# Kernel optimization log

Hardware: AMD Instinct MI355X
Metric: run time of the kernel (lower is better)

The kernel has to match this reference:

```python
import jax, jax.numpy as jnp
import numpy as np

SEQ_LEN = 2_097_152  # free sequence dimension
NUM_SYMBOLS = 10
NUM_STATES = 10
NUM_CLASSES = 2


def setup_inputs() -> dict:
    key = jax.random.key(0)
    k1, k2, k3, k4 = jax.random.split(key, 4)
    # x[t] is a probability distribution over symbols (soft one-hot), matching
    # the automaton semantics and keeping the 2M-step recurrence numerically stable.
    x = jax.random.uniform(k1, (SEQ_LEN, NUM_SYMBOLS), dtype=jnp.float32)
    x = x / jnp.sum(x, axis=1, keepdims=True)
    # Parameters, initialized exactly as in the torch module (__init__ softmaxes).
    P = jax.nn.softmax(jax.random.normal(k2, (NUM_SYMBOLS, NUM_STATES, NUM_STATES), dtype=jnp.float32), axis=2)
    start_state = jax.nn.softmax(jax.random.normal(k3, (NUM_STATES,), dtype=jnp.float32), axis=0)
    accept_states = jax.nn.softmax(jax.random.normal(k4, (NUM_STATES, NUM_CLASSES), dtype=jnp.float32), axis=1)
    return {"x": x, "P": P, "start_state": start_state, "accept_states": accept_states}


def reference(x, P, start_state, accept_states):
    # Sequential recurrence: s_{t+1} = s_t @ (sum_k x[t,k] * P[k])
    def step(s, xt):
        Wt = jnp.einsum('k,kij->ij', xt, P)  # [S, S] symbol-weighted transition
        return s @ Wt, None
    s, _ = jax.lax.scan(step, start_state, x)
    return s @ accept_states  # [num_classes]
```

## Files before the change

### kernel.cpp

```cpp
#include <hip/hip_runtime.h>

#define TEN 10

__global__ __attribute__((amdgpu_flat_work_group_size(256, 256),
                          amdgpu_waves_per_eu(1, 1)))
void automaton_chunks(const float* __restrict__ x, const float* __restrict__ P,
                      float* __restrict__ outBlk, long long T, int C)
{
    __shared__ __align__(16) float lds[8704];

    const int tid  = threadIdx.x;
    const int wave = tid >> 6;
    const int lane = tid & 63;
    const int grp  = lane / 5;
    const int sub  = lane % 5;
    const bool active = (grp < 12);
    const int cib  = wave * 12 + grp;
    const int j0 = 2 * sub, j1 = j0 + 1;

    float p[2][TEN][TEN];
    float m[TEN][2];
    long long Lc = 0;
    const float2* xp = nullptr;
    float* slot = lds + (active ? cib : 0) * 132;

    if (active) {
        const long long chunk = (long long)blockIdx.x * 48 + cib;
        const long long s0 = chunk * T / C;
        const long long s1 = (chunk + 1) * T / C;
        Lc = s1 - s0;
        xp = reinterpret_cast<const float2*>(x) + s0 * 5;
#pragma unroll
        for (int k = 0; k < TEN; ++k)
#pragma unroll
            for (int a = 0; a < TEN; ++a) {
                const float2 v = *reinterpret_cast<const float2*>(P + k * 100 + a * TEN + j0);
                p[0][k][a] = v.x;
                p[1][k][a] = v.y;
            }
#pragma unroll
        for (int r = 0; r < TEN; ++r) {
            m[r][0] = (r == j0) ? 1.0f : 0.0f;
            m[r][1] = (r == j1) ? 1.0f : 0.0f;
        }
    }

    float2 nx0, nx1, nx2, nx3, nx4;
    if (active) { nx0 = xp[0]; nx1 = xp[1]; nx2 = xp[2]; nx3 = xp[3]; nx4 = xp[4]; xp += 5; }

    if (active) {
#pragma unroll 1
        for (long long s = 0; s < Lc; ++s) {
            const float xv[TEN] = {nx0.x, nx0.y, nx1.x, nx1.y, nx2.x,
                                   nx2.y, nx3.x, nx3.y, nx4.x, nx4.y};
            if (s + 1 < Lc) {
                nx0 = xp[0]; nx1 = xp[1]; nx2 = xp[2]; nx3 = xp[3]; nx4 = xp[4];
                xp += 5;
            }

            {
                float* c0 = slot + j0 * 12;
                reinterpret_cast<float4*>(c0)[0] = make_float4(m[0][0], m[1][0], m[2][0], m[3][0]);
                reinterpret_cast<float4*>(c0)[1] = make_float4(m[4][0], m[5][0], m[6][0], m[7][0]);
                reinterpret_cast<float2*>(c0 + 8)[0] = make_float2(m[8][0], m[9][0]);
                float* c1 = slot + j1 * 12;
                reinterpret_cast<float4*>(c1)[0] = make_float4(m[0][1], m[1][1], m[2][1], m[3][1]);
                reinterpret_cast<float4*>(c1)[1] = make_float4(m[4][1], m[5][1], m[6][1], m[7][1]);
                reinterpret_cast<float2*>(c1 + 8)[0] = make_float2(m[8][1], m[9][1]);
            }
            __builtin_amdgcn_wave_barrier();

            float w0[TEN], w1[TEN];
#pragma unroll
            for (int a = 0; a < TEN; ++a) {
                float a0 = xv[0] * p[0][0][a];
                float a1 = xv[0] * p[1][0][a];
#pragma unroll
                for (int k = 1; k < TEN; ++k) {
                    a0 = fmaf(xv[k], p[0][k][a], a0);
                    a1 = fmaf(xv[k], p[1][k][a], a1);
                }
                w0[a] = a0; w1[a] = a1;
            }

            float mn[TEN][2];
#pragma unroll
            for (int r = 0; r < TEN; ++r) { mn[r][0] = 0.0f; mn[r][1] = 0.0f; }
#pragma unroll
            for (int a = 0; a < TEN; ++a) {
                const float4 v0 = reinterpret_cast<const float4*>(slot + a * 12)[0];
                const float4 v1 = reinterpret_cast<const float4*>(slot + a * 12)[1];
                const float2 v2 = reinterpret_cast<const float2*>(slot + a * 12 + 8)[0];
                const float ca[TEN] = {v0.x, v0.y, v0.z, v0.w, v1.x, v1.y, v1.z, v1.w, v2.x, v2.y};
                const float wa0 = w0[a], wa1 = w1[a];
#pragma unroll
                for (int r = 0; r < TEN; ++r) {
                    mn[r][0] = fmaf(ca[r], wa0, mn[r][0]);
                    mn[r][1] = fmaf(ca[r], wa1, mn[r][1]);
                }
            }
#pragma unroll
            for (int r = 0; r < TEN; ++r) { m[r][0] = mn[r][0]; m[r][1] = mn[r][1]; }
            __builtin_amdgcn_wave_barrier();
        }
    }

    __syncthreads();
    if (active) {
        float* t = lds + cib * 120;
#pragma unroll
        for (int r = 0; r < TEN; ++r) {
            t[r * 12 + j0] = m[r][0];
            t[r * 12 + j1] = m[r][1];
        }
    }
    __syncthreads();

    {
        const float* src = lds;
        float* dst = lds + 5760;
        int n = 48;
        while (n > 3) {
            const int np = n >> 1;
            const int pI = tid / TEN;
            const int r  = tid % TEN;
            if (pI < np) {
                const float* A = src + (2 * pI) * 120;
                const float* B = src + (2 * pI + 1) * 120;
                float ar[TEN];
#pragma unroll
                for (int j = 0; j < TEN; ++j) ar[j] = A[r * 12 + j];
                float c[TEN] = {0, 0, 0, 0, 0, 0, 0, 0, 0, 0};
#pragma unroll
                for (int a = 0; a < TEN; ++a) {
                    const float ma = ar[a];
#pragma unroll
                    for (int j = 0; j < TEN; ++j) c[j] = fmaf(ma, B[a * 12 + j], c[j]);
                }
                float* C = dst + pI * 120;
#pragma unroll
                for (int j = 0; j < TEN; ++j) C[r * 12 + j] = c[j];
            }
            __syncthreads();
            const float* ts = src; src = dst; dst = const_cast<float*>(ts);
            n = np;
        }
        if (tid < TEN) {
            const int r = tid;
            float ar[TEN];
#pragma unroll
            for (int j = 0; j < TEN; ++j) ar[j] = src[r * 12 + j];
            float c[TEN] = {0, 0, 0, 0, 0, 0, 0, 0, 0, 0};
#pragma unroll
            for (int a = 0; a < TEN; ++a) {
                const float ma = ar[a];
#pragma unroll
                for (int j = 0; j < TEN; ++j) c[j] = fmaf(ma, src[120 + a * 12 + j], c[j]);
            }
#pragma unroll
            for (int j = 0; j < TEN; ++j) lds[5760 + r * 12 + j] = c[j];
        }
        __syncthreads();
        if (tid < TEN) {
            const int r = tid;
            float c[TEN] = {0, 0, 0, 0, 0, 0, 0, 0, 0, 0};
#pragma unroll
            for (int a = 0; a < TEN; ++a) {
                const float ma = lds[5760 + r * 12 + a];
#pragma unroll
                for (int j = 0; j < TEN; ++j) c[j] = fmaf(ma, src[240 + a * 12 + j], c[j]);
            }
            float* dr = outBlk + (size_t)blockIdx.x * 100 + r * TEN;
#pragma unroll
            for (int j = 0; j < TEN; ++j) dr[j] = c[j];
        }
    }
}

__device__ __forceinline__ void tree64(float* lds, int tid)
{
    const int q     = tid >> 2;
    const int sub   = tid & 3;
    const int rbase = (sub == 3) ? 8 : sub * 3;
    const int r0 = rbase, r1 = rbase + 1;
    const int r2 = (rbase + 2 > 9) ? 9 : rbase + 2;
    const bool w2 = (sub < 2);

    for (int np = 32; np >= 1; np >>= 1) {
        float c[3][TEN];
        if (q < np) {
            const float* A = lds + (2 * q) * 120;
            const float* B = lds + (2 * q + 1) * 120;
            float ar[3][TEN];
#pragma unroll
            for (int t = 0; t < 3; ++t) {
                const int rt = (t == 0) ? r0 : (t == 1) ? r1 : r2;
                const float4 a0 = reinterpret_cast<const float4*>(A + rt * 12)[0];
                const float4 a1 = reinterpret_cast<const float4*>(A + rt * 12)[1];
                const float2 a2 = reinterpret_cast<const float2*>(A + rt * 12 + 8)[0];
                ar[t][0]=a0.x; ar[t][1]=a0.y; ar[t][2]=a0.z; ar[t][3]=a0.w;
                ar[t][4]=a1.x; ar[t][5]=a1.y; ar[t][6]=a1.z; ar[t][7]=a1.w;
                ar[t][8]=a2.x; ar[t][9]=a2.y;
#pragma unroll
                for (int j = 0; j < TEN; ++j) c[t][j] = 0.0f;
            }
#pragma unroll
            for (int a = 0; a < TEN; ++a) {
                const float4 b0 = reinterpret_cast<const float4*>(B + a * 12)[0];
                const float4 b1 = reinterpret_cast<const float4*>(B + a * 12)[1];
                const float2 b2 = reinterpret_cast<const float2*>(B + a * 12 + 8)[0];
                const float br[TEN] = {b0.x,b0.y,b0.z,b0.w,b1.x,b1.y,b1.z,b1.w,b2.x,b2.y};
#pragma unroll
                for (int t = 0; t < 3; ++t) {
                    const float ma = ar[t][a];
#pragma unroll
                    for (int j = 0; j < TEN; ++j) c[t][j] = fmaf(ma, br[j], c[t][j]);
                }
            }
        }
        __syncthreads();
        if (q < np) {
            float* C = lds + q * 120;
#pragma unroll
            for (int t = 0; t < 3; ++t) {
                const int rt = (t == 0) ? r0 : (t == 1) ? r1 : r2;
                if (t < 2 || w2) {
                    float* cr = C + rt * 12;
                    reinterpret_cast<float4*>(cr)[0] = make_float4(c[t][0], c[t][1], c[t][2], c[t][3]);
                    reinterpret_cast<float4*>(cr)[1] = make_float4(c[t][4], c[t][5], c[t][6], c[t][7]);
                    reinterpret_cast<float2*>(cr + 8)[0] = make_float2(c[t][8], c[t][9]);
                }
            }
        }
        __syncthreads();
    }
}

__global__ void automaton_final(const float* __restrict__ blkM,
                                const float* __restrict__ start,
                                const float* __restrict__ acc,
                                float* __restrict__ outv)
{
    __shared__ __align__(16) float lds[7680];
    __shared__ float sv[TEN];
    const int tid = threadIdx.x;
    const int q   = tid >> 2;
    const int sub = tid & 3;
    const int rbase = (sub == 3) ? 8 : sub * 3;
    const int rr0 = rbase, rr1 = rbase + 1;
    const int rr2 = (rbase + 2 > 9) ? 9 : rbase + 2;
    const bool w2 = (sub < 2);

    float a[3][TEN];
    {
        const int rr[3] = {rr0, rr1, rr2};
        const float* A0 = blkM + (size_t)(4 * q) * 100;
#pragma unroll
        for (int t = 0; t < 3; ++t) {
            const float2* pp = reinterpret_cast<const float2*>(A0 + rr[t] * TEN);
            const float2 a0 = pp[0], a1 = pp[1], a2 = pp[2], a3 = pp[3], a4 = pp[4];
            a[t][0]=a0.x; a[t][1]=a0.y; a[t][2]=a1.x; a[t][3]=a1.y; a[t][4]=a2.x;
            a[t][5]=a2.y; a[t][6]=a3.x; a[t][7]=a3.y; a[t][8]=a4.x; a[t][9]=a4.y;
        }
    }
#pragma unroll 1
    for (int i = 1; i < 4; ++i) {
        const float* B = blkM + (size_t)(4 * q + i) * 100;
        float c[3][TEN];
#pragma unroll
        for (int t = 0; t < 3; ++t)
#pragma unroll
            for (int j = 0; j < TEN; ++j) c[t][j] = 0.0f;
#pragma unroll
        for (int aa = 0; aa < TEN; ++aa) {
            const float2* br = reinterpret_cast<const float2*>(B + aa * TEN);
            const float2 b0 = br[0], b1 = br[1], b2 = br[2], b3 = br[3], b4 = br[4];
            const float bv[TEN] = {b0.x,b0.y,b1.x,b1.y,b2.x,b2.y,b3.x,b3.y,b4.x,b4.y};
#pragma unroll
            for (int t = 0; t < 3; ++t) {
                const float ma = a[t][aa];
#pragma unroll
                for (int j = 0; j < TEN; ++j) c[t][j] = fmaf(ma, bv[j], c[t][j]);
            }
        }
#pragma unroll
        for (int t = 0; t < 3; ++t)
#pragma unroll
            for (int j = 0; j < TEN; ++j) a[t][j] = c[t][j];
    }
    {
        float* dst = lds + q * 120;
#pragma unroll
        for (int t = 0; t < 3; ++t) {
            const int rt = (t == 0) ? rr0 : (t == 1) ? rr1 : rr2;
            if (t < 2 || w2) {
                float* dr = dst + rt * 12;
                reinterpret_cast<float4*>(dr)[0] = make_float4(a[t][0], a[t][1], a[t][2], a[t][3]);
                reinterpret_cast<float4*>(dr)[1] = make_float4(a[t][4], a[t][5], a[t][6], a[t][7]);
                reinterpret_cast<float2*>(dr + 8)[0] = make_float2(a[t][8], a[t][9]);
            }
        }
    }
    __syncthreads();
    tree64(lds, tid);

    if (tid < TEN) {
        const int j = tid;
        float v = 0.0f;
#pragma unroll
        for (int r = 0; r < TEN; ++r) v = fmaf(start[r], lds[r * 12 + j], v);
        sv[j] = v;
    }
    __syncthreads();
    if (tid == 0) {
        float o0 = 0.0f, o1 = 0.0f;
#pragma unroll
        for (int j = 0; j < TEN; ++j) {
            o0 = fmaf(sv[j], acc[2 * j + 0], o0);
            o1 = fmaf(sv[j], acc[2 * j + 1], o1);
        }
        outv[0] = o0;
        outv[1] = o1;
    }
}

extern "C" void kernel_launch(void* const* d_in, const int* in_sizes, int n_in,
                              void* d_out, int out_size, void* d_ws, size_t ws_size,
                              hipStream_t stream)
{
    const float* x     = (const float*)d_in[0];
    const float* P     = (const float*)d_in[1];
    const float* start = (const float*)d_in[2];
    const float* acc   = (const float*)d_in[3];
    float* out         = (float*)d_out;

    const long long T = (long long)in_sizes[0] / TEN;
    const int C = 12288;

    float* blkM = (float*)d_ws;

    automaton_chunks<<<256, 256, 0, stream>>>(x, P, blkM, T, C);
    automaton_final<<<1, 256, 0, stream>>>(blkM, start, acc, out);
}
```

Before: 267.0 us.

## Interleave two independent chunk recurrences per thread group for ILP

Each 5-lane group now processes two adjacent sequence chunks in lockstep, with separate LDS slots and registers for each, then merges them with one extra 10x10 product before the block reduction. The total chunk count doubles while the grid stays the same. The aim is to hide the LDS round-trip latency and the dependent FMA chains of the serial recurrence by interleaving two independent chains. The cost is roughly double register pressure for state, weights and prefetched inputs, plus a larger LDS footprint.

```diff
diff --git a/kernel.cpp b/kernel.cpp
--- a/kernel.cpp
+++ b/kernel.cpp
@@ -1,13 +1,56 @@
 #include <hip/hip_runtime.h>
 
 #define TEN 10
+
+
+#define PUBLISH(mREG, slot)                                                     \
+    {                                                                           \
+        float* c0_ = (slot) + j0 * 12;                                          \
+        reinterpret_cast<float4*>(c0_)[0] = make_float4(mREG[0][0], mREG[1][0], mREG[2][0], mREG[3][0]); \
+        reinterpret_cast<float4*>(c0_)[1] = make_float4(mREG[4][0], mREG[5][0], mREG[6][0], mREG[7][0]); \
+        reinterpret_cast<float2*>(c0_ + 8)[0] = make_float2(mREG[8][0], mREG[9][0]); \
+        float* c1_ = (slot) + j1 * 12;                                          \
+        reinterpret_cast<float4*>(c1_)[0] = make_float4(mREG[0][1], mREG[1][1], mREG[2][1], mREG[3][1]); \
+        reinterpret_cast<float4*>(c1_)[1] = make_float4(mREG[4][1], mREG[5][1], mREG[6][1], mREG[7][1]); \
+        reinterpret_cast<float2*>(c1_ + 8)[0] = make_float2(mREG[8][1], mREG[9][1]); \
+    }
+
+#define WBUILD(xv, w0, w1)                                                      \
+    _Pragma("unroll")                                                           \
+    for (int a = 0; a < TEN; ++a) {                                             \
+        float a0_ = (xv)[0] * p[0][0][a];                                       \
+        float a1_ = (xv)[0] * p[1][0][a];                                       \
+        _Pragma("unroll")                                                       \
+        for (int k = 1; k < TEN; ++k) {                                         \
+            a0_ = fmaf((xv)[k], p[0][k][a], a0_);                               \
+            a1_ = fmaf((xv)[k], p[1][k][a], a1_);                               \
+        }                                                                       \
+        (w0)[a] = a0_; (w1)[a] = a1_;                                           \
+    }
+
+#define STREAM(slot, w0, w1, mREG)                                              \
+    _Pragma("unroll")                                                           \
+    for (int a = 0; a < TEN; ++a) {                                             \
+        const float4 v0_ = reinterpret_cast<const float4*>((slot) + a * 12)[0]; \
+        const float4 v1_ = reinterpret_cast<const float4*>((slot) + a * 12)[1]; \
+        const float2 v2_ = reinterpret_cast<const float2*>((slot) + a * 12 + 8)[0]; \
+        const float ca_[TEN] = {v0_.x, v0_.y, v0_.z, v0_.w, v1_.x, v1_.y, v1_.z, v1_.w, v2_.x, v2_.y}; \
+        const float wa0_ = (w0)[a], wa1_ = (w1)[a];                             \
+        if (a == 0) {                                                           \
+            _Pragma("unroll")                                                   \
+            for (int r = 0; r < TEN; ++r) { mREG[r][0] = ca_[r] * wa0_; mREG[r][1] = ca_[r] * wa1_; } \
+        } else {                                                                \
+            _Pragma("unroll")                                                   \
+            for (int r = 0; r < TEN; ++r) { mREG[r][0] = fmaf(ca_[r], wa0_, mREG[r][0]); mREG[r][1] = fmaf(ca_[r], wa1_, mREG[r][1]); } \
+        }                                                                       \
+    }
 
 __global__ __attribute__((amdgpu_flat_work_group_size(256, 256),
                           amdgpu_waves_per_eu(1, 1)))
 void automaton_chunks(const float* __restrict__ x, const float* __restrict__ P,
                       float* __restrict__ outBlk, long long T, int C)
 {
-    __shared__ __align__(16) float lds[8704];
+    __shared__ __align__(16) float lds[12672];
 
     const int tid  = threadIdx.x;
     const int wave = tid >> 6;
@@ -15,21 +58,25 @@
     const int grp  = lane / 5;
     const int sub  = lane % 5;
     const bool active = (grp < 12);
-    const int cib  = wave * 12 + grp;
+    const int gib  = wave * 12 + grp;
     const int j0 = 2 * sub, j1 = j0 + 1;
 
     float p[2][TEN][TEN];
-    float m[TEN][2];
-    long long Lc = 0;
-    const float2* xp = nullptr;
-    float* slot = lds + (active ? cib : 0) * 132;
+    float mA[TEN][2], mB[TEN][2];
+    long long LA = 0, LB = 0;
+    const float2 *xpA = nullptr, *xpB = nullptr;
+    float* slotA = lds + (active ? gib : 0) * 132;
+    float* slotB = slotA + 6336;
 
     if (active) {
-        const long long chunk = (long long)blockIdx.x * 48 + cib;
-        const long long s0 = chunk * T / C;
-        const long long s1 = (chunk + 1) * T / C;
-        Lc = s1 - s0;
-        xp = reinterpret_cast<const float2*>(x) + s0 * 5;
+        const long long cA  = (long long)blockIdx.x * 96 + 2 * gib;
+        const long long sA0 = cA * T / C;
+        const long long sA1 = (cA + 1) * T / C;
+        const long long sB1 = (cA + 2) * T / C;
+        LA = sA1 - sA0;
+        LB = sB1 - sA1;
+        xpA = reinterpret_cast<const float2*>(x) + sA0 * 5;
+        xpB = reinterpret_cast<const float2*>(x) + sA1 * 5;
 #pragma unroll
         for (int k = 0; k < TEN; ++k)
 #pragma unroll
@@ -40,78 +87,87 @@
             }
 #pragma unroll
         for (int r = 0; r < TEN; ++r) {
-            m[r][0] = (r == j0) ? 1.0f : 0.0f;
-            m[r][1] = (r == j1) ? 1.0f : 0.0f;
-        }
-    }
-
-    float2 nx0, nx1, nx2, nx3, nx4;
-    if (active) { nx0 = xp[0]; nx1 = xp[1]; nx2 = xp[2]; nx3 = xp[3]; nx4 = xp[4]; xp += 5; }
-
+            mA[r][0] = (r == j0) ? 1.0f : 0.0f;
+            mA[r][1] = (r == j1) ? 1.0f : 0.0f;
+            mB[r][0] = mA[r][0];
+            mB[r][1] = mA[r][1];
+        }
+    }
+
+    float2 nA0, nA1, nA2, nA3, nA4, nB0, nB1, nB2, nB3, nB4;
     if (active) {
+        nA0 = xpA[0]; nA1 = xpA[1]; nA2 = xpA[2]; nA3 = xpA[3]; nA4 = xpA[4]; xpA += 5;
+        nB0 = xpB[0]; nB1 = xpB[1]; nB2 = xpB[2]; nB3 = xpB[3]; nB4 = xpB[4]; xpB += 5;
+    }
+
+    if (active) {
+        const long long smin = (LA < LB) ? LA : LB;
 #pragma unroll 1
-        for (long long s = 0; s < Lc; ++s) {
-            const float xv[TEN] = {nx0.x, nx0.y, nx1.x, nx1.y, nx2.x,
-                                   nx2.y, nx3.x, nx3.y, nx4.x, nx4.y};
-            if (s + 1 < Lc) {
-                nx0 = xp[0]; nx1 = xp[1]; nx2 = xp[2]; nx3 = xp[3]; nx4 = xp[4];
-                xp += 5;
-            }
-
-            {
-                float* c0 = slot + j0 * 12;
-                reinterpret_cast<float4*>(c0)[0] = make_float4(m[0][0], m[1][0], m[2][0], m[3][0]);
-                reinterpret_cast<float4*>(c0)[1] = make_float4(m[4][0], m[5][0], m[6][0], m[7][0]);
-                reinterpret_cast<float2*>(c0 + 8)[0] = make_float2(m[8][0], m[9][0]);
-                float* c1 = slot + j1 * 12;
-                reinterpret_cast<float4*>(c1)[0] = make_float4(m[0][1], m[1][1], m[2][1], m[3][1]);
-                reinterpret_cast<float4*>(c1)[1] = make_float4(m[4][1], m[5][1], m[6][1], m[7][1]);
-                reinterpret_cast<float2*>(c1 + 8)[0] = make_float2(m[8][1], m[9][1]);
-            }
-            __builtin_amdgcn_wave_barrier();
-
-            float w0[TEN], w1[TEN];
-#pragma unroll
-            for (int a = 0; a < TEN; ++a) {
-                float a0 = xv[0] * p[0][0][a];
-                float a1 = xv[0] * p[1][0][a];
-#pragma unroll
-                for (int k = 1; k < TEN; ++k) {
-                    a0 = fmaf(xv[k], p[0][k][a], a0);
-                    a1 = fmaf(xv[k], p[1][k][a], a1);
-                }
-                w0[a] = a0; w1[a] = a1;
-            }
-
-            float mn[TEN][2];
-#pragma unroll
-            for (int r = 0; r < TEN; ++r) { mn[r][0] = 0.0f; mn[r][1] = 0.0f; }
-#pragma unroll
-            for (int a = 0; a < TEN; ++a) {
-                const float4 v0 = reinterpret_cast<const float4*>(slot + a * 12)[0];
-                const float4 v1 = reinterpret_cast<const float4*>(slot + a * 12)[1];
-                const float2 v2 = reinterpret_cast<const float2*>(slot + a * 12 + 8)[0];
-                const float ca[TEN] = {v0.x, v0.y, v0.z, v0.w, v1.x, v1.y, v1.z, v1.w, v2.x, v2.y};
-                const float wa0 = w0[a], wa1 = w1[a];
-#pragma unroll
-                for (int r = 0; r < TEN; ++r) {
-                    mn[r][0] = fmaf(ca[r], wa0, mn[r][0]);
-                    mn[r][1] = fmaf(ca[r], wa1, mn[r][1]);
-                }
-            }
-#pragma unroll
-            for (int r = 0; r < TEN; ++r) { m[r][0] = mn[r][0]; m[r][1] = mn[r][1]; }
-            __builtin_amdgcn_wave_barrier();
+        for (long long s = 0; s < smin; ++s) {
+            const float xvA[TEN] = {nA0.x, nA0.y, nA1.x, nA1.y, nA2.x,
+                                    nA2.y, nA3.x, nA3.y, nA4.x, nA4.y};
+            const float xvB[TEN] = {nB0.x, nB0.y, nB1.x, nB1.y, nB2.x,
+                                    nB2.y, nB3.x, nB3.y, nB4.x, nB4.y};
+            if (s + 1 < LA) {
+                nA0 = xpA[0]; nA1 = xpA[1]; nA2 = xpA[2]; nA3 = xpA[3]; nA4 = xpA[4];
+                xpA += 5;
+            }
+            if (s + 1 < LB) {
+                nB0 = xpB[0]; nB1 = xpB[1]; nB2 = xpB[2]; nB3 = xpB[3]; nB4 = xpB[4];
+                xpB += 5;
+            }
+
+            PUBLISH(mA, slotA)
+            PUBLISH(mB, slotB)
+            __builtin_amdgcn_wave_barrier();
+
+            float wA0[TEN], wA1[TEN], wB0[TEN], wB1[TEN];
+            WBUILD(xvA, wA0, wA1)
+            WBUILD(xvB, wB0, wB1)
+
+            STREAM(slotA, wA0, wA1, mA)
+            STREAM(slotB, wB0, wB1, mB)
+            __builtin_amdgcn_wave_barrier();
+        }
+
+        if (LA > smin) {
+            const float xvA[TEN] = {nA0.x, nA0.y, nA1.x, nA1.y, nA2.x,
+                                    nA2.y, nA3.x, nA3.y, nA4.x, nA4.y};
+            PUBLISH(mA, slotA)
+            __builtin_amdgcn_wave_barrier();
+            float wA0[TEN], wA1[TEN];
+            WBUILD(xvA, wA0, wA1)
+            STREAM(slotA, wA0, wA1, mA)
+            __builtin_amdgcn_wave_barrier();
+        }
+        if (LB > smin) {
+            const float xvB[TEN] = {nB0.x, nB0.y, nB1.x, nB1.y, nB2.x,
+                                    nB2.y, nB3.x, nB3.y, nB4.x, nB4.y};
+            PUBLISH(mB, slotB)
+            __builtin_amdgcn_wave_barrier();
+            float wB0[TEN], wB1[TEN];
+            WBUILD(xvB, wB0, wB1)
+            STREAM(slotB, wB0, wB1, mB)
+            __builtin_amdgcn_wave_barrier();
+        }
+
+        {
+            PUBLISH(mA, slotA)
+            __builtin_amdgcn_wave_barrier();
+            float wA0[TEN], wA1[TEN];
+#pragma unroll
+            for (int a = 0; a < TEN; ++a) { wA0[a] = mB[a][0]; wA1[a] = mB[a][1]; }
+            STREAM(slotA, wA0, wA1, mA)
         }
     }
 
     __syncthreads();
     if (active) {
-        float* t = lds + cib * 120;
+        float* t = lds + gib * 120;
 #pragma unroll
         for (int r = 0; r < TEN; ++r) {
-            t[r * 12 + j0] = m[r][0];
-            t[r * 12 + j1] = m[r][1];
+            t[r * 12 + j0] = mA[r][0];
+            t[r * 12 + j1] = mA[r][1];
         }
     }
     __syncthreads();
@@ -137,9 +193,9 @@
 #pragma unroll
                     for (int j = 0; j < TEN; ++j) c[j] = fmaf(ma, B[a * 12 + j], c[j]);
                 }
-                float* C = dst + pI * 120;
-#pragma unroll
-                for (int j = 0; j < TEN; ++j) C[r * 12 + j] = c[j];
+                float* Cp = dst + pI * 120;
+#pragma unroll
+                for (int j = 0; j < TEN; ++j) Cp[r * 12 + j] = c[j];
             }
             __syncthreads();
             const float* ts = src; src = dst; dst = const_cast<float*>(ts);
@@ -335,7 +391,7 @@
     float* out         = (float*)d_out;
 
     const long long T = (long long)in_sizes[0] / TEN;
-    const int C = 12288;
+    const int C = 24576;
 
     float* blkM = (float*)d_ws;
 
```

Result: slower. 361.3 us (+35.3%).

## Share symbol-weighted matrices via double-buffered LDS and pipeline W build with update

Applied to the files above, without the earlier changes.

Reverses which operand goes through LDS. Each lane group now publishes its next step's weighted transition matrix W to shared memory, instead of sharing the running product columns. Each lane keeps two rows of the product in registers, and the LDS slot is double-buffered. This lets the W build for step s+1 overlap with the matrix update for step s, aiming to shorten the serial dependency chain per step. The cost is more LDS use and a transposed result layout, which also changes the final writeback.

```diff
diff --git a/kernel.cpp b/kernel.cpp
--- a/kernel.cpp
+++ b/kernel.cpp
@@ -1,13 +1,61 @@
 #include <hip/hip_runtime.h>
 
 #define TEN 10
+
+
+#define WBUILD(xv, w0, w1)                                                      \
+    _Pragma("unroll")                                                           \
+    for (int a = 0; a < TEN; ++a) {                                             \
+        float a0_ = (xv)[0] * p[0][0][a];                                       \
+        float a1_ = (xv)[0] * p[1][0][a];                                       \
+        _Pragma("unroll")                                                       \
+        for (int k = 1; k < TEN; ++k) {                                         \
+            a0_ = fmaf((xv)[k], p[0][k][a], a0_);                               \
+            a1_ = fmaf((xv)[k], p[1][k][a], a1_);                               \
+        }                                                                       \
+        (w0)[a] = a0_; (w1)[a] = a1_;                                           \
+    }
+
+#define PUBLISH_W(w0, w1, slot)                                                 \
+    {                                                                           \
+        float* c0_ = (slot) + j0 * 12;                                          \
+        reinterpret_cast<float4*>(c0_)[0] = make_float4((w0)[0], (w0)[1], (w0)[2], (w0)[3]); \
+        reinterpret_cast<float4*>(c0_)[1] = make_float4((w0)[4], (w0)[5], (w0)[6], (w0)[7]); \
+        reinterpret_cast<float2*>(c0_ + 8)[0] = make_float2((w0)[8], (w0)[9]);  \
+        float* c1_ = (slot) + j1 * 12;                                          \
+        reinterpret_cast<float4*>(c1_)[0] = make_float4((w1)[0], (w1)[1], (w1)[2], (w1)[3]); \
+        reinterpret_cast<float4*>(c1_)[1] = make_float4((w1)[4], (w1)[5], (w1)[6], (w1)[7]); \
+        reinterpret_cast<float2*>(c1_ + 8)[0] = make_float2((w1)[8], (w1)[9]);  \
+    }
+
+#define UPDATE(slot)                                                            \
+    {                                                                           \
+        float mn0[TEN], mn1[TEN];                                              \
+        _Pragma("unroll")                                                       \
+        for (int j = 0; j < TEN; ++j) {                                         \
+            const float4 v0_ = reinterpret_cast<const float4*>((slot) + j * 12)[0]; \
+            const float4 v1_ = reinterpret_cast<const float4*>((slot) + j * 12)[1]; \
+            const float2 v2_ = reinterpret_cast<const float2*>((slot) + j * 12 + 8)[0]; \
+            const float ca_[TEN] = {v0_.x, v0_.y, v0_.z, v0_.w, v1_.x, v1_.y, v1_.z, v1_.w, v2_.x, v2_.y}; \
+            float t0_ = m0[0] * ca_[0];                                         \
+            float t1_ = m1[0] * ca_[0];                                         \
+            _Pragma("unroll")                                                   \
+            for (int a = 1; a < TEN; ++a) {                                     \
+                t0_ = fmaf(m0[a], ca_[a], t0_);                                 \
+                t1_ = fmaf(m1[a], ca_[a], t1_);                                 \
+            }                                                                   \
+            mn0[j] = t0_; mn1[j] = t1_;                                         \
+        }                                                                       \
+        _Pragma("unroll")                                                       \
+        for (int j = 0; j < TEN; ++j) { m0[j] = mn0[j]; m1[j] = mn1[j]; }       \
+    }
 
 __global__ __attribute__((amdgpu_flat_work_group_size(256, 256),
                           amdgpu_waves_per_eu(1, 1)))
 void automaton_chunks(const float* __restrict__ x, const float* __restrict__ P,
                       float* __restrict__ outBlk, long long T, int C)
 {
-    __shared__ __align__(16) float lds[8704];
+    __shared__ __align__(16) float lds[12672];
 
     const int tid  = threadIdx.x;
     const int wave = tid >> 6;
@@ -15,17 +63,18 @@
     const int grp  = lane / 5;
     const int sub  = lane % 5;
     const bool active = (grp < 12);
-    const int cib  = wave * 12 + grp;
+    const int gib  = wave * 12 + grp;
     const int j0 = 2 * sub, j1 = j0 + 1;
 
     float p[2][TEN][TEN];
-    float m[TEN][2];
+    float m0[TEN], m1[TEN];
     long long Lc = 0;
     const float2* xp = nullptr;
-    float* slot = lds + (active ? cib : 0) * 132;
+    float* slotA = lds + (active ? gib : 0) * 132;
+    float* slotB = slotA + 6336;
 
     if (active) {
-        const long long chunk = (long long)blockIdx.x * 48 + cib;
+        const long long chunk = (long long)blockIdx.x * 48 + gib;
         const long long s0 = chunk * T / C;
         const long long s1 = (chunk + 1) * T / C;
         Lc = s1 - s0;
@@ -39,80 +88,62 @@
                 p[1][k][a] = v.y;
             }
 #pragma unroll
-        for (int r = 0; r < TEN; ++r) {
-            m[r][0] = (r == j0) ? 1.0f : 0.0f;
-            m[r][1] = (r == j1) ? 1.0f : 0.0f;
-        }
-    }
-
-    float2 nx0, nx1, nx2, nx3, nx4;
-    if (active) { nx0 = xp[0]; nx1 = xp[1]; nx2 = xp[2]; nx3 = xp[3]; nx4 = xp[4]; xp += 5; }
+        for (int j = 0; j < TEN; ++j) {
+            m0[j] = (j == j0) ? 1.0f : 0.0f;
+            m1[j] = (j == j1) ? 1.0f : 0.0f;
+        }
+    }
 
     if (active) {
+        float2 nx0 = xp[0], nx1 = xp[1], nx2 = xp[2], nx3 = xp[3], nx4 = xp[4];
+        xp += 5;
+
+        {
+            const float xv[TEN] = {nx0.x, nx0.y, nx1.x, nx1.y, nx2.x,
+                                   nx2.y, nx3.x, nx3.y, nx4.x, nx4.y};
+            if (Lc > 1) {
+                nx0 = xp[0]; nx1 = xp[1]; nx2 = xp[2]; nx3 = xp[3]; nx4 = xp[4];
+                xp += 5;
+            }
+            float w0[TEN], w1[TEN];
+            WBUILD(xv, w0, w1)
+            PUBLISH_W(w0, w1, slotA)
+        }
+        __builtin_amdgcn_wave_barrier();
+
+        float* cur = slotA;
+        float* nxt = slotB;
 #pragma unroll 1
         for (long long s = 0; s < Lc; ++s) {
-            const float xv[TEN] = {nx0.x, nx0.y, nx1.x, nx1.y, nx2.x,
-                                   nx2.y, nx3.x, nx3.y, nx4.x, nx4.y};
-            if (s + 1 < Lc) {
-                nx0 = xp[0]; nx1 = xp[1]; nx2 = xp[2]; nx3 = xp[3]; nx4 = xp[4];
-                xp += 5;
-            }
-
-            {
-                float* c0 = slot + j0 * 12;
-                reinterpret_cast<float4*>(c0)[0] = make_float4(m[0][0], m[1][0], m[2][0], m[3][0]);
-                reinterpret_cast<float4*>(c0)[1] = make_float4(m[4][0], m[5][0], m[6][0], m[7][0]);
-                reinterpret_cast<float2*>(c0 + 8)[0] = make_float2(m[8][0], m[9][0]);
-                float* c1 = slot + j1 * 12;
-                reinterpret_cast<float4*>(c1)[0] = make_float4(m[0][1], m[1][1], m[2][1], m[3][1]);
-                reinterpret_cast<float4*>(c1)[1] = make_float4(m[4][1], m[5][1], m[6][1], m[7][1]);
-                reinterpret_cast<float2*>(c1 + 8)[0] = make_float2(m[8][1], m[9][1]);
-            }
+            const bool more = (s + 1 < Lc);
+            float w0[TEN], w1[TEN];
+            if (more) {
+                const float xv[TEN] = {nx0.x, nx0.y, nx1.x, nx1.y, nx2.x,
+                                       nx2.y, nx3.x, nx3.y, nx4.x, nx4.y};
+                if (s + 2 < Lc) {
+                    nx0 = xp[0]; nx1 = xp[1]; nx2 = xp[2]; nx3 = xp[3]; nx4 = xp[4];
+                    xp += 5;
+                }
+                WBUILD(xv, w0, w1)
+            }
+            UPDATE(cur)
+            if (more) PUBLISH_W(w0, w1, nxt)
             __builtin_amdgcn_wave_barrier();
-
-            float w0[TEN], w1[TEN];
-#pragma unroll
-            for (int a = 0; a < TEN; ++a) {
-                float a0 = xv[0] * p[0][0][a];
-                float a1 = xv[0] * p[1][0][a];
-#pragma unroll
-                for (int k = 1; k < TEN; ++k) {
-                    a0 = fmaf(xv[k], p[0][k][a], a0);
-                    a1 = fmaf(xv[k], p[1][k][a], a1);
-                }
-                w0[a] = a0; w1[a] = a1;
-            }
-
-            float mn[TEN][2];
-#pragma unroll
-            for (int r = 0; r < TEN; ++r) { mn[r][0] = 0.0f; mn[r][1] = 0.0f; }
-#pragma unroll
-            for (int a = 0; a < TEN; ++a) {
-                const float4 v0 = reinterpret_cast<const float4*>(slot + a * 12)[0];
-                const float4 v1 = reinterpret_cast<const float4*>(slot + a * 12)[1];
-                const float2 v2 = reinterpret_cast<const float2*>(slot + a * 12 + 8)[0];
-                const float ca[TEN] = {v0.x, v0.y, v0.z, v0.w, v1.x, v1.y, v1.z, v1.w, v2.x, v2.y};
-                const float wa0 = w0[a], wa1 = w1[a];
-#pragma unroll
-                for (int r = 0; r < TEN; ++r) {
-                    mn[r][0] = fmaf(ca[r], wa0, mn[r][0]);
-                    mn[r][1] = fmaf(ca[r], wa1, mn[r][1]);
-                }
-            }
-#pragma unroll
-            for (int r = 0; r < TEN; ++r) { m[r][0] = mn[r][0]; m[r][1] = mn[r][1]; }
-            __builtin_amdgcn_wave_barrier();
+            float* t = cur; cur = nxt; nxt = t;
         }
     }
 
     __syncthreads();
     if (active) {
-        float* t = lds + cib * 120;
-#pragma unroll
-        for (int r = 0; r < TEN; ++r) {
-            t[r * 12 + j0] = m[r][0];
-            t[r * 12 + j1] = m[r][1];
-        }
+        float* t = lds + gib * 120;
+        float* r0p = t + j0 * 12;
+        reinterpret_cast<float4*>(r0p)[0] = make_float4(m0[0], m0[1], m0[2], m0[3]);
+        reinterpret_cast<float4*>(r0p)[1] = make_float4(m0[4], m0[5], m0[6], m0[7]);
+        reinterpret_cast<float2*>(r0p + 8)[0] = make_float2(m0[8], m0[9]);
+        float* r1p = t + j1 * 12;
+        reinterpret_cast<float4*>(r1p)[0] = make_float4(m1[0], m1[1], m1[2], m1[3]);
+        reinterpret_cast<float4*>(r1p)[1] = make_float4(m1[4], m1[5], m1[6], m1[7]);
+        reinterpret_cast<float2*>(r1p + 8)[0] = make_float2(m1[8], m1[9]);
     }
     __syncthreads();
 
@@ -137,9 +168,9 @@
 #pragma unroll
                     for (int j = 0; j < TEN; ++j) c[j] = fmaf(ma, B[a * 12 + j], c[j]);
                 }
-                float* C = dst + pI * 120;
-#pragma unroll
-                for (int j = 0; j < TEN; ++j) C[r * 12 + j] = c[j];
+                float* Cp = dst + pI * 120;
+#pragma unroll
+                for (int j = 0; j < TEN; ++j) Cp[r * 12 + j] = c[j];
             }
             __syncthreads();
             const float* ts = src; src = dst; dst = const_cast<float*>(ts);
```

Result: slower. 305.0 us (+14.2%).
